# Kernel tuning notes

Measured on AMD Instinct MI355X. Metric: run time of the kernel, lower is better.

## Reference

```python
import jax, jax.numpy as jnp
import numpy as np

D_MODEL = 512
HEAD = 64

def setup_inputs() -> dict:
    key = jax.random.key(0)
    ks = jax.random.split(key, 7)
    s_in = 1.0 / np.sqrt(D_MODEL)
    x = jax.random.normal(ks[0], (4, 4096, D_MODEL), dtype=jnp.float32)
    Wk = jax.random.uniform(ks[1], (D_MODEL, HEAD), jnp.float32, -s_in, s_in)
    bk = jax.random.uniform(ks[2], (HEAD,), jnp.float32, -s_in, s_in)
    Wq = jax.random.uniform(ks[3], (D_MODEL, HEAD), jnp.float32, -s_in, s_in)
    bq = jax.random.uniform(ks[4], (HEAD,), jnp.float32, -s_in, s_in)
    Wv = jax.random.uniform(ks[5], (D_MODEL, HEAD), jnp.float32, -s_in, s_in)
    bv = jax.random.uniform(ks[6], (HEAD,), jnp.float32, -s_in, s_in)
    return {"x": x, "Wk": Wk, "bk": bk, "Wq": Wq, "bq": bq, "Wv": Wv, "bv": bv}

def reference(x, Wk, bk, Wq, bq, Wv, bv):
    B, T, C = x.shape
    k = x @ Wk + bk            # [B,T,H]
    q = x @ Wq + bq            # [B,T,H]
    v = x @ Wv + bv            # [B,T,H]
    scale = C ** (-0.5)
    # NOTE: original computes k @ q^T (keys index rows), softmax over query axis
    w = jnp.einsum('bkh,bqh->bkq', k, q) * scale  # [B,T,T]
    w = jax.nn.softmax(w, axis=-1)
    out = jnp.einsum('bkq,bqh->bkh', w, v)        # [B,T,H]
    return out
```

## Files before the change

### kernel.cpp

```cpp
#include <hip/hip_runtime.h>


#define DM 512
#define HD 64
#define TSEQ 4096
#define KSCALE (1.4426950408889634f * 0.04419417382415922f)

typedef __attribute__((ext_vector_type(8))) __bf16 bf16x8;
typedef __attribute__((ext_vector_type(4))) __bf16 bf16x4;
typedef __attribute__((ext_vector_type(2))) __bf16 bf16x2;
typedef __attribute__((ext_vector_type(4))) float f32x4;
typedef __attribute__((ext_vector_type(16))) float f32x16;
typedef __attribute__((ext_vector_type(4))) unsigned int uint4v;

__device__ __forceinline__ float fast_exp2(float x) {
#if __has_builtin(__builtin_amdgcn_exp2f)
    return __builtin_amdgcn_exp2f(x);
#else
    return exp2f(x);
#endif
}

__device__ __forceinline__ bf16x8 ld_bf16x8(const unsigned short* p) {
    return __builtin_bit_cast(bf16x8, *(const uint4v*)p);
}
__device__ __forceinline__ f32x4 mfma16(bf16x8 a, bf16x8 b, f32x4 c) {
    return __builtin_amdgcn_mfma_f32_16x16x32_bf16(a, b, c, 0, 0, 0);
}
__device__ __forceinline__ f32x16 mfma32(bf16x8 a, bf16x8 b, f32x16 c) {
    return __builtin_amdgcn_mfma_f32_32x32x16_bf16(a, b, c, 0, 0, 0);
}

typedef const __attribute__((address_space(1))) unsigned int* gas_t;
typedef __attribute__((address_space(3))) unsigned int* las_t;
__device__ __forceinline__ void async_cp16(const void* g, void* l) {
    __builtin_amdgcn_global_load_lds((gas_t)(unsigned long long)g,
                                     (las_t)(unsigned int)(unsigned long long)l,
                                     16, 0, 0);
}

__global__ __launch_bounds__(256) void prep_wt(const float* __restrict__ Wk,
                                               const float* __restrict__ Wq,
                                               const float* __restrict__ Wv,
                                               unsigned short* __restrict__ WT) {
    int e = blockIdx.x * 256 + threadIdx.x;
    int m = e >> 15;
    int idx = e & 32767;
    int h = idx >> 9;
    int cc = idx & 511;
    const float* W = (m == 0) ? Wk : ((m == 1) ? Wq : Wv);
    float v = W[cc * HD + h];
    if (m == 0) v *= KSCALE;
    ((__bf16*)WT)[m * 32768 + h * DM + cc] = (__bf16)v;
}

__global__ __launch_bounds__(512, 4) void proj(const float* __restrict__ x,
                                               const unsigned short* __restrict__ WT,
                                               const float* __restrict__ bk,
                                               const float* __restrict__ bq,
                                               const float* __restrict__ bv,
                                               unsigned short* __restrict__ Kw,
                                               unsigned short* __restrict__ Qw,
                                               unsigned short* __restrict__ VTw) {
    __shared__ alignas(16) float xs[16384];
    const int tid = threadIdx.x;
    const int wv = tid >> 6, lane = tid & 63;
    const int c = lane & 15, quad = lane >> 4;
    const int ng = wv & 3, rg = wv >> 2;
    const int bx = blockIdx.x;
    const int n0 = ng * 16;

#pragma unroll
    for (int r = 0; r < 8; ++r) {
        int cid = r * 512 + tid;
        int row = cid >> 7, pos = cid & 127;
        int g = (pos & ~7) | ((pos ^ row) & 7);
        async_cp16((const char*)x + (size_t)(bx * 32 + row) * 2048 + g * 16,
                   (char*)xs + r * 8192 + wv * 1024);
    }
    __builtin_amdgcn_s_waitcnt(0x0f70);
    __syncthreads();

    const int arow = rg * 16 + c;
    const unsigned short* wtb = WT + (n0 + c) * DM + quad * 8;
    f32x4 acc[3];
#pragma unroll
    for (int m = 0; m < 3; ++m) acc[m] = (f32x4){0.f, 0.f, 0.f, 0.f};

#pragma unroll
    for (int ks = 0; ks < 16; ++ks) {
        int p0 = ks * 8 + quad * 2;
        int sp0 = (p0 & ~7) | ((p0 ^ arow) & 7);
        int sp1 = ((p0 + 1) & ~7) | (((p0 + 1) ^ arow) & 7);
        f32x4 xa = *(const f32x4*)((const char*)xs + arow * 2048 + sp0 * 16);
        f32x4 xb = *(const f32x4*)((const char*)xs + arow * 2048 + sp1 * 16);
        bf16x8 af;
        af[0] = (__bf16)xa[0]; af[1] = (__bf16)xa[1]; af[2] = (__bf16)xa[2]; af[3] = (__bf16)xa[3];
        af[4] = (__bf16)xb[0]; af[5] = (__bf16)xb[1]; af[6] = (__bf16)xb[2]; af[7] = (__bf16)xb[3];
#pragma unroll
        for (int m = 0; m < 3; ++m) {
            bf16x8 bf = ld_bf16x8(wtb + m * 32768 + ks * 32);
            acc[m] = mfma16(af, bf, acc[m]);
        }
    }

    const int row0 = bx * 32 + rg * 16 + quad * 4;
#pragma unroll
    for (int m = 0; m < 3; ++m) {
        const float* bp = (m == 0) ? bk : ((m == 1) ? bq : bv);
        float bias = bp[n0 + c];
        if (m == 0) bias *= KSCALE;
        if (m < 2) {
            __bf16* dst = (__bf16*)((m == 0) ? Kw : Qw);
#pragma unroll
            for (int r = 0; r < 4; ++r)
                dst[(row0 + r) * HD + n0 + c] = (__bf16)(acc[m][r] + bias);
        } else {
            bf16x4 pk;
#pragma unroll
            for (int r = 0; r < 4; ++r) pk[r] = (__bf16)(acc[m][r] + bias);
            int b = bx >> 7;
            int rowb = (bx & 127) * 32 + rg * 16 + quad * 4;
            *(bf16x4*)(VTw + ((size_t)(b * 64 + n0 + c)) * TSEQ + rowb) = pk;
        }
    }
}

__global__ __launch_bounds__(512, 2) void attn(const unsigned short* __restrict__ Kw,
                                               const unsigned short* __restrict__ Qw,
                                               const unsigned short* __restrict__ VTw,
                                               float* __restrict__ Op,
                                               float* __restrict__ Lp) {
    __shared__ alignas(16) char smem[65536];

    const int tid = threadIdx.x;
    const int wv = tid >> 6, lane = tid & 63;
    const int l5 = lane >> 5, l31 = lane & 31;
    const int rg = wv >> 2, jc = wv & 3;
    const int bx = blockIdx.x;
    const int lb = (bx & 7) * 32 + (bx >> 3);
    const int batch = lb >> 6, js = (lb >> 5) & 1, tile = lb & 31;
    const int rowbase = batch * TSEQ + tile * 128;

    bf16x8 kf[2][4];
#pragma unroll
    for (int it = 0; it < 2; ++it) {
        const unsigned short* kp = Kw + (size_t)(rowbase + rg * 64 + it * 32 + l31) * HD;
#pragma unroll
        for (int ks = 0; ks < 4; ++ks) kf[it][ks] = ld_bf16x8(kp + ks * 16 + l5 * 8);
    }

    const int jrow = jc * 32 + l31;
    int qoff[4];
#pragma unroll
    for (int ks = 0; ks < 4; ++ks)
        qoff[ks] = jrow * 128 + (((ks * 2 + l5) ^ (jrow & 7)) * 16);
    int voff[2][2];
#pragma unroll
    for (int ht = 0; ht < 2; ++ht)
#pragma unroll
        for (int k2 = 0; k2 < 2; ++k2) {
            int h = ht * 32 + l31;
            voff[ht][k2] = h * 256 + (((jc * 4 + k2 * 2 + l5) ^ (h & 15)) * 16);
        }

    const char* qg = (const char*)(Qw + (size_t)(batch * TSEQ + js * 2048) * HD);
    const char* vg = (const char*)(VTw + (size_t)batch * 64 * TSEQ + js * 2048);
    const int L1 = 512 + tid;
    const int qgo0 = ((tid >> 3) * 128) + (((tid & 7) ^ ((tid >> 3) & 7)) * 16);
    const int qgo1 = ((L1 >> 3) * 128) + (((L1 & 7) ^ ((L1 >> 3) & 7)) * 16);
    const int vgo0 = ((tid >> 4) * 8192) + (((tid & 15) ^ ((tid >> 4) & 15)) * 16);
    const int vgo1 = ((L1 >> 4) * 8192) + (((L1 & 15) ^ ((L1 >> 4) & 15)) * 16);

    f32x16 o00, o01, o10, o11;
#pragma unroll
    for (int r = 0; r < 16; ++r) { o00[r] = 0.f; o01[r] = 0.f; o10[r] = 0.f; o11[r] = 0.f; }
    float lac0 = 0.f, lac1 = 0.f;

    {
        char* nb = smem;
        async_cp16(qg + qgo0, nb + wv * 1024);
        async_cp16(qg + qgo1, nb + 8192 + wv * 1024);
        async_cp16(vg + vgo0, nb + 16384 + wv * 1024);
        async_cp16(vg + vgo1, nb + 16384 + 8192 + wv * 1024);
    }

    for (int jt = 0; jt < 16; ++jt) {
        __builtin_amdgcn_s_waitcnt(0x0f70);
        __syncthreads();
        const char* cb = smem + (jt & 1) * 32768;
        if (jt < 15) {
            char* nb = smem + ((jt + 1) & 1) * 32768;
            async_cp16(qg + (jt + 1) * 16384 + qgo0, nb + wv * 1024);
            async_cp16(qg + (jt + 1) * 16384 + qgo1, nb + 8192 + wv * 1024);
            async_cp16(vg + (jt + 1) * 256 + vgo0, nb + 16384 + wv * 1024);
            async_cp16(vg + (jt + 1) * 256 + vgo1, nb + 16384 + 8192 + wv * 1024);
            __builtin_amdgcn_sched_barrier(0);
        }
        const unsigned short* QL = (const unsigned short*)cb;
        const unsigned short* VL = (const unsigned short*)(cb + 16384);

        f32x16 s0, s1;
#pragma unroll
        for (int r = 0; r < 16; ++r) { s0[r] = 0.f; s1[r] = 0.f; }
#pragma unroll
        for (int ks = 0; ks < 4; ++ks) {
            bf16x8 qa = ld_bf16x8((const unsigned short*)((const char*)QL + qoff[ks]));
            s0 = mfma32(qa, kf[0][ks], s0);
            s1 = mfma32(qa, kf[1][ks], s1);
        }

        unsigned int pk0[8], pk1[8];
#pragma unroll
        for (int m = 0; m < 8; ++m) {
            float a0 = fast_exp2(s0[2 * m]), a1 = fast_exp2(s0[2 * m + 1]);
            float b0 = fast_exp2(s1[2 * m]), b1 = fast_exp2(s1[2 * m + 1]);
            lac0 += a0 + a1;
            lac1 += b0 + b1;
            bf16x2 ta; ta[0] = (__bf16)a0; ta[1] = (__bf16)a1;
            bf16x2 tb; tb[0] = (__bf16)b0; tb[1] = (__bf16)b1;
            pk0[m] = __builtin_bit_cast(unsigned int, ta);
            pk1[m] = __builtin_bit_cast(unsigned int, tb);
        }

#pragma unroll
        for (int k2 = 0; k2 < 2; ++k2) {
            bf16x8 pb0, pb1;
            {
                unsigned int A0 = pk0[k2 * 4 + 0], A1 = pk0[k2 * 4 + 1];
                unsigned int B0 = pk0[k2 * 4 + 2], B1 = pk0[k2 * 4 + 3];
                unsigned int t0 = l5 ? A0 : B0, t1 = l5 ? A1 : B1;
                unsigned int r0 = (unsigned int)__shfl_xor((int)t0, 32, 64);
                unsigned int r1 = (unsigned int)__shfl_xor((int)t1, 32, 64);
                uint4v u;
                u[0] = l5 ? r0 : A0; u[1] = l5 ? r1 : A1;
                u[2] = l5 ? B0 : r0; u[3] = l5 ? B1 : r1;
                pb0 = __builtin_bit_cast(bf16x8, u);
            }
            {
                unsigned int A0 = pk1[k2 * 4 + 0], A1 = pk1[k2 * 4 + 1];
                unsigned int B0 = pk1[k2 * 4 + 2], B1 = pk1[k2 * 4 + 3];
                unsigned int t0 = l5 ? A0 : B0, t1 = l5 ? A1 : B1;
                unsigned int r0 = (unsigned int)__shfl_xor((int)t0, 32, 64);
                unsigned int r1 = (unsigned int)__shfl_xor((int)t1, 32, 64);
                uint4v u;
                u[0] = l5 ? r0 : A0; u[1] = l5 ? r1 : A1;
                u[2] = l5 ? B0 : r0; u[3] = l5 ? B1 : r1;
                pb1 = __builtin_bit_cast(bf16x8, u);
            }
            bf16x8 vf0 = ld_bf16x8((const unsigned short*)((const char*)VL + voff[0][k2]));
            bf16x8 vf1 = ld_bf16x8((const unsigned short*)((const char*)VL + voff[1][k2]));
            o00 = mfma32(vf0, pb0, o00);
            o01 = mfma32(vf0, pb1, o01);
            o10 = mfma32(vf1, pb0, o10);
            o11 = mfma32(vf1, pb1, o11);
        }
    }

    lac0 += __shfl_xor(lac0, 32, 64);
    lac1 += __shfl_xor(lac1, 32, 64);
    __syncthreads();
    float* OCp = (float*)smem;
    float* ldsl = (float*)(smem + 34816);
    if (l5 == 0) {
        ldsl[jc * 128 + rg * 64 + l31] = lac0;
        ldsl[jc * 128 + rg * 64 + 32 + l31] = lac1;
    }

#pragma unroll
    for (int ph = 0; ph < 4; ++ph) {
        const int ht = ph >> 1, ih = ph & 1;
        __syncthreads();
        if (rg == ih) {
            const f32x16 oa = ht ? o10 : o00;
            const f32x16 ob = ht ? o11 : o01;
#pragma unroll
            for (int r = 0; r < 16; ++r) {
                int hr = (r & 3) + 8 * (r >> 2) + 4 * l5;
                OCp[(jc * 32 + hr) * 68 + l31] = oa[r];
                OCp[(jc * 32 + hr) * 68 + 32 + l31] = ob[r];
            }
        }
        __syncthreads();
#pragma unroll
        for (int rep = 0; rep < 4; ++rep) {
            int idx = rep * 512 + tid;
            int i = idx >> 5, hr = idx & 31;
            float v = OCp[(0 * 32 + hr) * 68 + i] + OCp[(1 * 32 + hr) * 68 + i]
                    + OCp[(2 * 32 + hr) * 68 + i] + OCp[(3 * 32 + hr) * 68 + i];
            Op[(size_t)js * 1048576 + (size_t)(rowbase + ih * 64 + i) * HD + ht * 32 + hr] = v;
        }
        if (ph == 0 && tid < 128) {
            float L = ldsl[tid] + ldsl[128 + tid] + ldsl[256 + tid] + ldsl[384 + tid];
            Lp[js * 16384 + rowbase + tid] = L;
        }
    }
}

__global__ __launch_bounds__(512) void fin(const float* __restrict__ Op,
                                           const float* __restrict__ Lp,
                                           float* __restrict__ out) {
    int idx = blockIdx.x * 512 + threadIdx.x;
    int e = idx * 4;
    int row = e >> 6;
    f32x4 a = *(const f32x4*)(Op + e);
    f32x4 b = *(const f32x4*)(Op + 1048576 + e);
    float L = Lp[row] + Lp[16384 + row];
    f32x4 r;
#pragma unroll
    for (int k = 0; k < 4; ++k) r[k] = (a[k] + b[k]) / L;
    *(f32x4*)(out + e) = r;
}

extern "C" void kernel_launch(void* const* d_in, const int* in_sizes, int n_in,
                              void* d_out, int out_size, void* d_ws, size_t ws_size,
                              hipStream_t stream) {
    (void)in_sizes; (void)n_in; (void)out_size; (void)ws_size;
    const float* x  = (const float*)d_in[0];
    const float* Wk = (const float*)d_in[1];
    const float* bk = (const float*)d_in[2];
    const float* Wq = (const float*)d_in[3];
    const float* bq = (const float*)d_in[4];
    const float* Wv = (const float*)d_in[5];
    const float* bv = (const float*)d_in[6];

    char* ws = (char*)d_ws;
    unsigned short* WT  = (unsigned short*)(ws);
    unsigned short* Kw  = (unsigned short*)(ws + 196608);
    unsigned short* Qw  = (unsigned short*)(ws + 2293760);
    unsigned short* VTw = (unsigned short*)(ws + 4390912);
    float* Opart        = (float*)(ws + 6488064);
    float* Lpart        = (float*)(ws + 14876672);
    float* outp = (float*)d_out;

    hipLaunchKernelGGL(prep_wt, dim3(384), dim3(256), 0, stream, Wk, Wq, Wv, WT);
    hipLaunchKernelGGL(proj, dim3(512), dim3(512), 0, stream,
                       x, WT, bk, bq, bv, Kw, Qw, VTw);
    hipLaunchKernelGGL(attn, dim3(256), dim3(512), 0, stream, Kw, Qw, VTw, Opart, Lpart);
    hipLaunchKernelGGL(fin, dim3(512), dim3(512), 0, stream, Opart, Lpart, outp);
}
```

Baseline: 136.4 us.

## Load V directly from global into registers and use permlane32 swap

V tiles are no longer staged through LDS with async copies. Each wave now loads its own V fragments straight from global memory at the start of every iteration, which halves the shared memory buffer. The cross-half shuffle of softmax probabilities is also replaced by the permlane32_swap builtin when it is available. The aim is less LDS traffic and footprint and cheaper lane exchange, at the cost of global load latency that is not prefetched and sits on the critical path before the PV MFMAs.

```diff
diff --git a/kernel.cpp b/kernel.cpp
--- a/kernel.cpp
+++ b/kernel.cpp
@@ -29,6 +29,21 @@
 }
 __device__ __forceinline__ f32x16 mfma32(bf16x8 a, bf16x8 b, f32x16 c) {
     return __builtin_amdgcn_mfma_f32_32x32x16_bf16(a, b, c, 0, 0, 0);
+}
+
+struct u32pair { unsigned int x, y; };
+__device__ __forceinline__ u32pair half_merge(unsigned int a, unsigned int b, int l5) {
+    u32pair p;
+#if __has_builtin(__builtin_amdgcn_permlane32_swap)
+    auto r = __builtin_amdgcn_permlane32_swap(a, b, false, false);
+    p.x = r[0]; p.y = r[1];
+#else
+    unsigned int t = l5 ? a : b;
+    unsigned int s = (unsigned int)__shfl_xor((int)t, 32, 64);
+    p.x = l5 ? s : a;
+    p.y = l5 ? b : s;
+#endif
+    return p;
 }
 
 typedef const __attribute__((address_space(1))) unsigned int* gas_t;
@@ -131,7 +146,7 @@
                                                const unsigned short* __restrict__ VTw,
                                                float* __restrict__ Op,
                                                float* __restrict__ Lp) {
-    __shared__ alignas(16) char smem[65536];
+    __shared__ alignas(16) char smem[36864];
 
     const int tid = threadIdx.x;
     const int wv = tid >> 6, lane = tid & 63;
@@ -155,22 +170,15 @@
 #pragma unroll
     for (int ks = 0; ks < 4; ++ks)
         qoff[ks] = jrow * 128 + (((ks * 2 + l5) ^ (jrow & 7)) * 16);
-    int voff[2][2];
-#pragma unroll
-    for (int ht = 0; ht < 2; ++ht)
-#pragma unroll
-        for (int k2 = 0; k2 < 2; ++k2) {
-            int h = ht * 32 + l31;
-            voff[ht][k2] = h * 256 + (((jc * 4 + k2 * 2 + l5) ^ (h & 15)) * 16);
-        }
+
+    const unsigned short* vrow0 = VTw + (size_t)(batch * 64 + l31) * TSEQ
+                                  + js * 2048 + jc * 32 + l5 * 8;
+    const unsigned short* vrow1 = vrow0 + (size_t)32 * TSEQ;
 
     const char* qg = (const char*)(Qw + (size_t)(batch * TSEQ + js * 2048) * HD);
-    const char* vg = (const char*)(VTw + (size_t)batch * 64 * TSEQ + js * 2048);
     const int L1 = 512 + tid;
     const int qgo0 = ((tid >> 3) * 128) + (((tid & 7) ^ ((tid >> 3) & 7)) * 16);
     const int qgo1 = ((L1 >> 3) * 128) + (((L1 & 7) ^ ((L1 >> 3) & 7)) * 16);
-    const int vgo0 = ((tid >> 4) * 8192) + (((tid & 15) ^ ((tid >> 4) & 15)) * 16);
-    const int vgo1 = ((L1 >> 4) * 8192) + (((L1 & 15) ^ ((L1 >> 4) & 15)) * 16);
 
     f32x16 o00, o01, o10, o11;
 #pragma unroll
@@ -181,24 +189,24 @@
         char* nb = smem;
         async_cp16(qg + qgo0, nb + wv * 1024);
         async_cp16(qg + qgo1, nb + 8192 + wv * 1024);
-        async_cp16(vg + vgo0, nb + 16384 + wv * 1024);
-        async_cp16(vg + vgo1, nb + 16384 + 8192 + wv * 1024);
     }
 
     for (int jt = 0; jt < 16; ++jt) {
         __builtin_amdgcn_s_waitcnt(0x0f70);
         __syncthreads();
-        const char* cb = smem + (jt & 1) * 32768;
+        const char* cb = smem + (jt & 1) * 16384;
         if (jt < 15) {
-            char* nb = smem + ((jt + 1) & 1) * 32768;
+            char* nb = smem + ((jt + 1) & 1) * 16384;
             async_cp16(qg + (jt + 1) * 16384 + qgo0, nb + wv * 1024);
             async_cp16(qg + (jt + 1) * 16384 + qgo1, nb + 8192 + wv * 1024);
-            async_cp16(vg + (jt + 1) * 256 + vgo0, nb + 16384 + wv * 1024);
-            async_cp16(vg + (jt + 1) * 256 + vgo1, nb + 16384 + 8192 + wv * 1024);
             __builtin_amdgcn_sched_barrier(0);
         }
         const unsigned short* QL = (const unsigned short*)cb;
-        const unsigned short* VL = (const unsigned short*)(cb + 16384);
+
+        bf16x8 v00 = ld_bf16x8(vrow0 + jt * 128);
+        bf16x8 v01 = ld_bf16x8(vrow0 + jt * 128 + 16);
+        bf16x8 v10 = ld_bf16x8(vrow1 + jt * 128);
+        bf16x8 v11 = ld_bf16x8(vrow1 + jt * 128 + 16);
 
         f32x16 s0, s1;
 #pragma unroll
@@ -227,29 +235,21 @@
         for (int k2 = 0; k2 < 2; ++k2) {
             bf16x8 pb0, pb1;
             {
-                unsigned int A0 = pk0[k2 * 4 + 0], A1 = pk0[k2 * 4 + 1];
-                unsigned int B0 = pk0[k2 * 4 + 2], B1 = pk0[k2 * 4 + 3];
-                unsigned int t0 = l5 ? A0 : B0, t1 = l5 ? A1 : B1;
-                unsigned int r0 = (unsigned int)__shfl_xor((int)t0, 32, 64);
-                unsigned int r1 = (unsigned int)__shfl_xor((int)t1, 32, 64);
+                u32pair p0 = half_merge(pk0[k2 * 4 + 0], pk0[k2 * 4 + 2], l5);
+                u32pair p1 = half_merge(pk0[k2 * 4 + 1], pk0[k2 * 4 + 3], l5);
                 uint4v u;
-                u[0] = l5 ? r0 : A0; u[1] = l5 ? r1 : A1;
-                u[2] = l5 ? B0 : r0; u[3] = l5 ? B1 : r1;
+                u[0] = p0.x; u[1] = p1.x; u[2] = p0.y; u[3] = p1.y;
                 pb0 = __builtin_bit_cast(bf16x8, u);
             }
             {
-                unsigned int A0 = pk1[k2 * 4 + 0], A1 = pk1[k2 * 4 + 1];
-                unsigned int B0 = pk1[k2 * 4 + 2], B1 = pk1[k2 * 4 + 3];
-                unsigned int t0 = l5 ? A0 : B0, t1 = l5 ? A1 : B1;
-                unsigned int r0 = (unsigned int)__shfl_xor((int)t0, 32, 64);
-                unsigned int r1 = (unsigned int)__shfl_xor((int)t1, 32, 64);
+                u32pair p0 = half_merge(pk1[k2 * 4 + 0], pk1[k2 * 4 + 2], l5);
+                u32pair p1 = half_merge(pk1[k2 * 4 + 1], pk1[k2 * 4 + 3], l5);
                 uint4v u;
-                u[0] = l5 ? r0 : A0; u[1] = l5 ? r1 : A1;
-                u[2] = l5 ? B0 : r0; u[3] = l5 ? B1 : r1;
+                u[0] = p0.x; u[1] = p1.x; u[2] = p0.y; u[3] = p1.y;
                 pb1 = __builtin_bit_cast(bf16x8, u);
             }
-            bf16x8 vf0 = ld_bf16x8((const unsigned short*)((const char*)VL + voff[0][k2]));
-            bf16x8 vf1 = ld_bf16x8((const unsigned short*)((const char*)VL + voff[1][k2]));
+            bf16x8 vf0 = k2 ? v01 : v00;
+            bf16x8 vf1 = k2 ? v11 : v10;
             o00 = mfma32(vf0, pb0, o00);
             o01 = mfma32(vf0, pb1, o01);
             o10 = mfma32(vf1, pb0, o10);
```

Result: slower. 142.5 us (+4.5%).

## Double attention block size to 16 waves with 256-row tiles per stage

Applied to the files above, without the earlier changes.

Grows the attention workgroup from 8 to 16 waves: each stage now stages 256 query/value rows in a 128KB double buffer and runs 8 stages instead of 16. The eight column groups split each tile, and their partial outputs and sums are reduced across 8 slices in LDS at the end. The aim is to halve the number of barrier-separated pipeline steps and give the scheduler more waves to hide latency. In exchange, 128KB of LDS per block probably allows only one block per CU, the cross-wave reduction gets larger, and the launch-bounds hint of 4 may squeeze registers.

```diff
diff --git a/kernel.cpp b/kernel.cpp
--- a/kernel.cpp
+++ b/kernel.cpp
@@ -126,17 +126,17 @@
     }
 }
 
-__global__ __launch_bounds__(512, 2) void attn(const unsigned short* __restrict__ Kw,
-                                               const unsigned short* __restrict__ Qw,
-                                               const unsigned short* __restrict__ VTw,
-                                               float* __restrict__ Op,
-                                               float* __restrict__ Lp) {
-    __shared__ alignas(16) char smem[65536];
+__global__ __launch_bounds__(1024, 4) void attn(const unsigned short* __restrict__ Kw,
+                                                const unsigned short* __restrict__ Qw,
+                                                const unsigned short* __restrict__ VTw,
+                                                float* __restrict__ Op,
+                                                float* __restrict__ Lp) {
+    __shared__ alignas(16) char smem[131072];
 
     const int tid = threadIdx.x;
     const int wv = tid >> 6, lane = tid & 63;
     const int l5 = lane >> 5, l31 = lane & 31;
-    const int rg = wv >> 2, jc = wv & 3;
+    const int rg = wv >> 3, jc = wv & 7;
     const int bx = blockIdx.x;
     const int lb = (bx & 7) * 32 + (bx >> 3);
     const int batch = lb >> 6, js = (lb >> 5) & 1, tile = lb & 31;
@@ -161,44 +161,44 @@
 #pragma unroll
         for (int k2 = 0; k2 < 2; ++k2) {
             int h = ht * 32 + l31;
-            voff[ht][k2] = h * 256 + (((jc * 4 + k2 * 2 + l5) ^ (h & 15)) * 16);
+            int wc = jc * 4 + k2 * 2 + l5;
+            voff[ht][k2] = h * 512 + (((wc & 16) | ((wc ^ h) & 15)) * 16);
         }
 
     const char* qg = (const char*)(Qw + (size_t)(batch * TSEQ + js * 2048) * HD);
-    const char* vg = (const char*)(VTw + (size_t)batch * 64 * TSEQ + js * 2048);
-    const int L1 = 512 + tid;
-    const int qgo0 = ((tid >> 3) * 128) + (((tid & 7) ^ ((tid >> 3) & 7)) * 16);
-    const int qgo1 = ((L1 >> 3) * 128) + (((L1 & 7) ^ ((L1 >> 3) & 7)) * 16);
-    const int vgo0 = ((tid >> 4) * 8192) + (((tid & 15) ^ ((tid >> 4) & 15)) * 16);
-    const int vgo1 = ((L1 >> 4) * 8192) + (((L1 & 15) ^ ((L1 >> 4) & 15)) * 16);
+    const char* vg = (const char*)(VTw + (size_t)batch * 64 * TSEQ) + js * 4096;
+    const int c1 = 1024 + tid;
+    const int qgo0 = ((tid >> 3) * 128) + ((((tid & 7) ^ (tid >> 3)) & 7) * 16);
+    const int qgo1 = ((c1 >> 3) * 128) + ((((c1 & 7) ^ (c1 >> 3)) & 7) * 16);
+    const int vgo0 = ((tid >> 5) * 8192)
+                   + (((tid & 16) | (((tid & 15) ^ (tid >> 5)) & 15)) * 16);
+    const int vgo1 = vgo0 + 32 * 8192;
 
     f32x16 o00, o01, o10, o11;
 #pragma unroll
     for (int r = 0; r < 16; ++r) { o00[r] = 0.f; o01[r] = 0.f; o10[r] = 0.f; o11[r] = 0.f; }
     float lac0 = 0.f, lac1 = 0.f;
 
-    {
-        char* nb = smem;
-        async_cp16(qg + qgo0, nb + wv * 1024);
-        async_cp16(qg + qgo1, nb + 8192 + wv * 1024);
-        async_cp16(vg + vgo0, nb + 16384 + wv * 1024);
-        async_cp16(vg + vgo1, nb + 16384 + 8192 + wv * 1024);
-    }
-
-    for (int jt = 0; jt < 16; ++jt) {
+    auto STAGE = [&](int t) {
+        char* nb = smem + (t & 1) * 65536;
+        async_cp16(qg + t * 32768 + qgo0, nb + wv * 1024);
+        async_cp16(qg + t * 32768 + qgo1, nb + 16384 + wv * 1024);
+        async_cp16(vg + t * 512 + vgo0, nb + 32768 + wv * 1024);
+        async_cp16(vg + t * 512 + vgo1, nb + 49152 + wv * 1024);
+    };
+
+    STAGE(0);
+
+    for (int jt = 0; jt < 8; ++jt) {
         __builtin_amdgcn_s_waitcnt(0x0f70);
         __syncthreads();
-        const char* cb = smem + (jt & 1) * 32768;
-        if (jt < 15) {
-            char* nb = smem + ((jt + 1) & 1) * 32768;
-            async_cp16(qg + (jt + 1) * 16384 + qgo0, nb + wv * 1024);
-            async_cp16(qg + (jt + 1) * 16384 + qgo1, nb + 8192 + wv * 1024);
-            async_cp16(vg + (jt + 1) * 256 + vgo0, nb + 16384 + wv * 1024);
-            async_cp16(vg + (jt + 1) * 256 + vgo1, nb + 16384 + 8192 + wv * 1024);
+        const char* cb = smem + (jt & 1) * 65536;
+        if (jt < 7) {
+            STAGE(jt + 1);
             __builtin_amdgcn_sched_barrier(0);
         }
         const unsigned short* QL = (const unsigned short*)cb;
-        const unsigned short* VL = (const unsigned short*)(cb + 16384);
+        const unsigned short* VL = (const unsigned short*)(cb + 32768);
 
         f32x16 s0, s1;
 #pragma unroll
@@ -261,7 +261,7 @@
     lac1 += __shfl_xor(lac1, 32, 64);
     __syncthreads();
     float* OCp = (float*)smem;
-    float* ldsl = (float*)(smem + 34816);
+    float* ldsl = (float*)(smem + 69632);
     if (l5 == 0) {
         ldsl[jc * 128 + rg * 64 + l31] = lac0;
         ldsl[jc * 128 + rg * 64 + 32 + l31] = lac1;
@@ -283,15 +283,18 @@
         }
         __syncthreads();
 #pragma unroll
-        for (int rep = 0; rep < 4; ++rep) {
-            int idx = rep * 512 + tid;
+        for (int rep = 0; rep < 2; ++rep) {
+            int idx = rep * 1024 + tid;
             int i = idx >> 5, hr = idx & 31;
-            float v = OCp[(0 * 32 + hr) * 68 + i] + OCp[(1 * 32 + hr) * 68 + i]
-                    + OCp[(2 * 32 + hr) * 68 + i] + OCp[(3 * 32 + hr) * 68 + i];
+            float v = 0.f;
+#pragma unroll
+            for (int j = 0; j < 8; ++j) v += OCp[(j * 32 + hr) * 68 + i];
             Op[(size_t)js * 1048576 + (size_t)(rowbase + ih * 64 + i) * HD + ht * 32 + hr] = v;
         }
         if (ph == 0 && tid < 128) {
-            float L = ldsl[tid] + ldsl[128 + tid] + ldsl[256 + tid] + ldsl[384 + tid];
+            float L = 0.f;
+#pragma unroll
+            for (int j = 0; j < 8; ++j) L += ldsl[j * 128 + tid];
             Lp[js * 16384 + rowbase + tid] = L;
         }
     }
@@ -336,6 +339,6 @@
     hipLaunchKernelGGL(prep_wt, dim3(384), dim3(256), 0, stream, Wk, Wq, Wv, WT);
     hipLaunchKernelGGL(proj, dim3(512), dim3(512), 0, stream,
                        x, WT, bk, bq, bv, Kw, Qw, VTw);
-    hipLaunchKernelGGL(attn, dim3(256), dim3(512), 0, stream, Kw, Qw, VTw, Opart, Lpart);
+    hipLaunchKernelGGL(attn, dim3(256), dim3(1024), 0, stream, Kw, Qw, VTw, Opart, Lpart);
     hipLaunchKernelGGL(fin, dim3(512), dim3(512), 0, stream, Opart, Lpart, outp);
 }
```

Result: slower. 187.0 us (+37.1%).
